# Optimization experiments

Hardware: AMD Instinct MI355X
Metric: run time of the kernel (lower is better)

Reference implementation:

```python
import jax, jax.numpy as jnp
import numpy as np

D_MODEL = 512
D_STATE = 16
D_CONV = 4
EXPAND = 2
D_INNER = EXPAND * D_MODEL  # 1024
DT_RANK = (D_MODEL + 15) // 16  # 32
BATCH = 8
SEQ = 1024
LN_EPS = 1e-5


def setup_inputs() -> dict:
    key = jax.random.key(0)
    ks = jax.random.split(key, 8)
    s = 0.02
    return {
        "x": jax.random.normal(ks[0], (BATCH, SEQ, D_MODEL), jnp.float32),
        "ln_g": jnp.ones((D_MODEL,), jnp.float32),
        "ln_b": jnp.zeros((D_MODEL,), jnp.float32),
        "in_proj_w": (jax.random.normal(ks[1], (2 * D_INNER, D_MODEL), jnp.float32) * s),
        "conv_w": (jax.random.normal(ks[2], (D_INNER, 1, D_CONV), jnp.float32) * s),
        "conv_b": jnp.zeros((D_INNER,), jnp.float32),
        "x_proj_w": (jax.random.normal(ks[3], (DT_RANK + 2 * D_STATE, D_INNER), jnp.float32) * s),
        "dt_proj_w": (jax.random.normal(ks[4], (D_INNER, DT_RANK), jnp.float32) * s),
        "dt_proj_b": jnp.full((D_INNER,), -4.0, jnp.float32),  # softplus(-4) ~ small init dt
        "A_log": jnp.log(jnp.broadcast_to(jnp.arange(1, D_STATE + 1, dtype=jnp.float32), (D_INNER, D_STATE))).copy(),
        "D": jnp.ones((D_INNER,), jnp.float32),
        "out_proj_w": (jax.random.normal(ks[5], (D_MODEL, D_INNER), jnp.float32) * s),
    }


def _block(x, ln_g, ln_b, in_proj_w, conv_w, conv_b, x_proj_w,
           dt_proj_w, dt_proj_b, A_log, D, out_proj_w):
    # Pre-norm (LayerNorm over last dim)
    mu = jnp.mean(x, axis=-1, keepdims=True)
    var = jnp.mean(jnp.square(x - mu), axis=-1, keepdims=True)
    xn = (x - mu) * jax.lax.rsqrt(var + LN_EPS) * ln_g + ln_b

    # in_proj -> (u, z), each [B, L, d_inner]
    xz = jnp.einsum('bld,ed->ble', xn, in_proj_w)
    u, z = jnp.split(xz, 2, axis=-1)

    # causal depthwise conv1d over L, then SiLU
    uc = jnp.transpose(u, (0, 2, 1))  # [B, di, L]
    uc = jax.lax.conv_general_dilated(
        uc, conv_w, window_strides=(1,), padding=[(D_CONV - 1, 0)],
        dimension_numbers=('NCH', 'OIH', 'NCH'), feature_group_count=D_INNER)
    uc = jax.nn.silu(uc + conv_b[None, :, None])
    uct = jnp.transpose(uc, (0, 2, 1))  # [B, L, di]

    # input-dependent SSM params
    x_dbl = jnp.einsum('bld,ed->ble', uct, x_proj_w)
    dt, Bt, Ct = jnp.split(x_dbl, [DT_RANK, DT_RANK + D_STATE], axis=-1)
    delta = jax.nn.softplus(jnp.einsum('blr,dr->bld', dt, dt_proj_w) + dt_proj_b)
    A = -jnp.exp(A_log)  # [di, ds]

    # selective scan over L; carry h: [B, di, ds]
    def step(h, ins):
        d_t, b_t, c_t, u_t = ins  # [B,di], [B,ds], [B,ds], [B,di]
        dA = jnp.exp(d_t[:, :, None] * A)
        h = dA * h + (d_t * u_t)[:, :, None] * b_t[:, None, :]
        y = jnp.einsum('bds,bs->bd', h, c_t)
        return h, y

    h0 = jnp.zeros((x.shape[0], D_INNER, D_STATE), x.dtype)
    xs = (jnp.swapaxes(delta, 0, 1), jnp.swapaxes(Bt, 0, 1),
          jnp.swapaxes(Ct, 0, 1), jnp.swapaxes(uct, 0, 1))
    _, ys = jax.lax.scan(step, h0, xs)
    y = jnp.swapaxes(ys, 0, 1) + uct * D  # [B, L, di]

    y = y * jax.nn.silu(z)
    out = jnp.einsum('bld,ed->ble', y, out_proj_w)
    # dropout in eval mode = identity; residual add
    return x + out


def reference(x, ln_g, ln_b, in_proj_w, conv_w, conv_b, x_proj_w,
              dt_proj_w, dt_proj_b, A_log, D, out_proj_w):
    return _block(x, ln_g, ln_b, in_proj_w, conv_w, conv_b, x_proj_w,
                  dt_proj_w, dt_proj_b, A_log, D, out_proj_w)
```

## Files before the change

### kernel.cpp

```cpp
#include <hip/hip_runtime.h>
#include <stdint.h>

#define BATCH 8
#define SEQ   1024
#define DM    512
#define DI    1024
#define DS    16
#define DTR   32
#define ROWS  (BATCH*SEQ)
#define NC    64
#define CL    16

typedef float  f32x4  __attribute__((ext_vector_type(4)));
typedef float  f32x2  __attribute__((ext_vector_type(2)));
typedef short  s16x8  __attribute__((ext_vector_type(8)));
typedef short  s16x4  __attribute__((ext_vector_type(4)));

__device__ __forceinline__ float b2f(uint16_t u) {
  union { uint32_t u; float f; } v; v.u = ((uint32_t)u) << 16; return v.f;
}
__device__ __forceinline__ uint16_t f2b(float f) {
  union { float f; uint32_t u; } v; v.f = f;
  uint32_t u = v.u;
  return (uint16_t)((u + 0x7FFFu + ((u >> 16) & 1u)) >> 16);
}

__device__ __forceinline__ void gload_lds16(const uint16_t* g, uint16_t* l) {
  __builtin_amdgcn_global_load_lds(
      (const __attribute__((address_space(1))) void*)g,
      (__attribute__((address_space(3))) void*)l, 16, 0, 0);
}

__device__ __forceinline__ void pow_tree2(float p, f32x2 a2[8]) {
  float p2 = p*p;
  f32x2 pp = {p2, p2};
  a2[0] = (f32x2){p, p2};
  a2[1] = a2[0]*pp;
  a2[2] = a2[1]*pp;
  a2[3] = a2[2]*pp;
  a2[4] = a2[3]*pp;
  a2[5] = a2[4]*pp;
  a2[6] = a2[5]*pp;
  a2[7] = a2[6]*pp;
}

#define CVT_N  ((2*DI*DM + (DTR+2*DS)*DI + DI*DTR + DM*DI)/4)
#define CVTB   (CVT_N/256)

__global__ __launch_bounds__(256) void cvt_ln(
    const float* __restrict__ s0, uint16_t* __restrict__ d0,
    const float* __restrict__ s1, uint16_t* __restrict__ d1,
    const float* __restrict__ s2, uint16_t* __restrict__ d2,
    const float* __restrict__ s3, uint16_t* __restrict__ d3,
    const float* __restrict__ x, const float* __restrict__ g,
    const float* __restrict__ bt, uint16_t* __restrict__ xn) {
  if (blockIdx.x < CVTB) {
    const int n0 = 2*DI*DM/4, n1 = (DTR+2*DS)*DI/4, n2 = DI*DTR/4;
    int i = blockIdx.x * 256 + threadIdx.x;
    const float* src; uint16_t* dst;
    if      (i < n0)          { src = s0; dst = d0; }
    else if (i < n0+n1)       { src = s1; dst = d1; i -= n0; }
    else if (i < n0+n1+n2)    { src = s2; dst = d2; i -= n0+n1; }
    else                      { src = s3; dst = d3; i -= n0+n1+n2; }
    f32x4 v = ((const f32x4*)src)[i];
    s16x4 o;
#pragma unroll
    for (int j = 0; j < 4; j++) o[j] = (short)f2b(v[j]);
    ((s16x4*)dst)[i] = o;
    return;
  }
  int w = threadIdx.x >> 6, lane = threadIdx.x & 63;
  int row = (blockIdx.x - CVTB) * 4 + w;
  const float* xr = x + (size_t)row * DM + lane * 8;
  f32x4 v0 = *(const f32x4*)xr;
  f32x4 v1 = *(const f32x4*)(xr + 4);
  float f[8]; float sacc = 0.f, sacc2 = 0.f;
#pragma unroll
  for (int i = 0; i < 4; i++) { f[i] = v0[i]; f[i+4] = v1[i]; }
#pragma unroll
  for (int i = 0; i < 8; i++) { sacc += f[i]; sacc2 += f[i]*f[i]; }
#pragma unroll
  for (int o = 32; o; o >>= 1) { sacc += __shfl_xor(sacc, o); sacc2 += __shfl_xor(sacc2, o); }
  float mu  = sacc * (1.f/DM);
  float var = sacc2 * (1.f/DM) - mu*mu;
  float rs  = rsqrtf(var + 1e-5f);
  f32x4 g0 = *(const f32x4*)(g + lane*8), g1 = *(const f32x4*)(g + lane*8 + 4);
  f32x4 b0 = *(const f32x4*)(bt + lane*8), b1 = *(const f32x4*)(bt + lane*8 + 4);
  float gg[8], bb[8];
#pragma unroll
  for (int i = 0; i < 4; i++) { gg[i] = g0[i]; gg[i+4] = g1[i]; bb[i] = b0[i]; bb[i+4] = b1[i]; }
  s16x8 o8;
#pragma unroll
  for (int i = 0; i < 8; i++) {
    float r = (f[i]-mu)*rs*gg[i] + bb[i];
    o8[i] = (short)f2b(r);
  }
  *(s16x8*)(xn + (size_t)row*DM + lane*8) = o8;
}

__device__ __forceinline__ void gemm128(
    const uint16_t* __restrict__ A, const uint16_t* __restrict__ B,
    int K, f32x4 acc[4][4], uint16_t* lA, uint16_t* lB) {
  int tid = threadIdx.x;
  int lane = tid & 63, w = tid >> 6;
  int wy = w >> 1, wx = w & 1;
  int quad = lane >> 4, l16 = lane & 15;
  int srow = tid >> 2;
  int scol = (tid & 3) ^ (srow & 3);
  const uint16_t* Ag0 = A + (size_t)(blockIdx.x*128 + srow)*K + scol*8;
  const uint16_t* Ag1 = Ag0 + (size_t)64*K;
  const uint16_t* Bg0 = B + (size_t)(blockIdx.y*128 + srow)*K + scol*8;
  const uint16_t* Bg1 = Bg0 + (size_t)64*K;
  uint16_t* lAp0 = lA + tid*8;
  uint16_t* lAp1 = lA + 2048 + tid*8;
  uint16_t* lBp0 = lB + tid*8;
  uint16_t* lBp1 = lB + 2048 + tid*8;
  int pa = quad ^ (l16 & 3);
  const uint16_t* afrag = lA + (wy*64 + l16)*32 + pa*8;
  const uint16_t* bfrag = lB + (wx*64 + l16)*32 + pa*8;
#pragma unroll
  for (int mt=0; mt<4; mt++)
#pragma unroll
  for (int nt=0; nt<4; nt++) acc[mt][nt] = (f32x4){0.f,0.f,0.f,0.f};
  for (int k0 = 0; k0 < K; k0 += 32) {
    __syncthreads();
    gload_lds16(Ag0 + k0, lAp0);
    gload_lds16(Ag1 + k0, lAp1);
    gload_lds16(Bg0 + k0, lBp0);
    gload_lds16(Bg1 + k0, lBp1);
    __syncthreads();
    s16x8 af[4], bf[4];
#pragma unroll
    for (int i=0;i<4;i++) {
      af[i] = *(const s16x8*)(afrag + i*16*32);
      bf[i] = *(const s16x8*)(bfrag + i*16*32);
    }
#pragma unroll
    for (int mt=0; mt<4; mt++)
#pragma unroll
    for (int nt=0; nt<4; nt++)
      acc[mt][nt] = __builtin_amdgcn_mfma_f32_16x16x32_bf16(af[mt], bf[nt], acc[mt][nt], 0,0,0);
  }
}

#define EPI128_IDX \
  int tid = threadIdx.x; int lane = tid & 63, w = tid >> 6; \
  int wy = w >> 1, wx = w & 1; int quad = lane >> 4, l16 = lane & 15;

__global__ __launch_bounds__(256) void gemm_inproj(
    const uint16_t* __restrict__ xn, const uint16_t* __restrict__ W,
    uint16_t* __restrict__ u, uint16_t* __restrict__ z) {
  __shared__ __align__(16) uint16_t lA[128*32];
  __shared__ __align__(16) uint16_t lB[128*32];
  f32x4 acc[4][4];
  gemm128(xn, W, DM, acc, lA, lB);
  EPI128_IDX
#pragma unroll
  for (int mt=0; mt<4; mt++)
#pragma unroll
  for (int nt=0; nt<4; nt++)
#pragma unroll
  for (int i=0; i<4; i++) {
    int gr = blockIdx.x*128 + wy*64 + mt*16 + quad*4 + i;
    int gc = blockIdx.y*128 + wx*64 + nt*16 + l16;
    float v = acc[mt][nt][i];
    if (gc < DI) u[(size_t)gr*DI + gc] = f2b(v);
    else         z[(size_t)gr*DI + (gc - DI)] = f2b(v);
  }
}

__global__ __launch_bounds__(256) void gemm_outproj(
    const uint16_t* __restrict__ yb, const uint16_t* __restrict__ W,
    const float* __restrict__ x, float* __restrict__ out) {
  __shared__ __align__(16) uint16_t lA[128*32];
  __shared__ __align__(16) uint16_t lB[128*32];
  f32x4 acc[4][4];
  gemm128(yb, W, DI, acc, lA, lB);
  EPI128_IDX
#pragma unroll
  for (int mt=0; mt<4; mt++)
#pragma unroll
  for (int nt=0; nt<4; nt++)
#pragma unroll
  for (int i=0; i<4; i++) {
    int gr = blockIdx.x*128 + wy*64 + mt*16 + quad*4 + i;
    int gc = blockIdx.y*128 + wx*64 + nt*16 + l16;
    out[(size_t)gr*DM + gc] = acc[mt][nt][i] + x[(size_t)gr*DM + gc];
  }
}

#define LSTR 40

__device__ __forceinline__ void gemm_tile(
    const uint16_t* __restrict__ A, const uint16_t* __restrict__ B,
    int ld, int kLen, int bx, f32x4 acc[2][2]) {
  __shared__ __align__(16) uint16_t lA[64*LSTR];
  __shared__ __align__(16) uint16_t lB[64*LSTR];
  int tid  = threadIdx.x;
  int lane = tid & 63, w = tid >> 6;
  int wy = w >> 1, wx = w & 1;
  int quad = lane >> 4, l16 = lane & 15;
  int sr = tid >> 2, sc = (tid & 3) << 3;
  const uint16_t* Ag = A + (size_t)(bx*64 + sr)*ld + sc;
  const uint16_t* Bg = B + (size_t)sr*ld + sc;
  uint16_t* lAw = &lA[sr*LSTR + sc];
  uint16_t* lBw = &lB[sr*LSTR + sc];
  const uint16_t* ap = &lA[(wy*32 + l16)*LSTR + quad*8];
  const uint16_t* bp = &lB[(wx*32 + l16)*LSTR + quad*8];
  f32x4 zero = {0.f,0.f,0.f,0.f};
  acc[0][0]=zero; acc[0][1]=zero; acc[1][0]=zero; acc[1][1]=zero;
  for (int k0 = 0; k0 < kLen; k0 += 32) {
    s16x8 av = *(const s16x8*)(Ag + k0);
    s16x8 bv = *(const s16x8*)(Bg + k0);
    __syncthreads();
    *(s16x8*)lAw = av;
    *(s16x8*)lBw = bv;
    __syncthreads();
    s16x8 a0 = *(const s16x8*)ap;
    s16x8 a1 = *(const s16x8*)(ap + 16*LSTR);
    s16x8 b0 = *(const s16x8*)bp;
    s16x8 b1 = *(const s16x8*)(bp + 16*LSTR);
    acc[0][0] = __builtin_amdgcn_mfma_f32_16x16x32_bf16(a0, b0, acc[0][0], 0,0,0);
    acc[0][1] = __builtin_amdgcn_mfma_f32_16x16x32_bf16(a0, b1, acc[0][1], 0,0,0);
    acc[1][0] = __builtin_amdgcn_mfma_f32_16x16x32_bf16(a1, b0, acc[1][0], 0,0,0);
    acc[1][1] = __builtin_amdgcn_mfma_f32_16x16x32_bf16(a1, b1, acc[1][1], 0,0,0);
  }
}

__global__ __launch_bounds__(256) void gemm_xproj_sk(
    const uint16_t* __restrict__ uct, const uint16_t* __restrict__ W,
    float* __restrict__ xpart) {
  f32x4 acc[2][2];
  int ks = blockIdx.y;
  gemm_tile(uct + ks*256, W + ks*256, DI, 256, blockIdx.x, acc);
  int tid = threadIdx.x; int lane = tid & 63, w = tid >> 6;
  int wy = w >> 1, wx = w & 1; int quad = lane >> 4, l16 = lane & 15;
  float* out = xpart + (size_t)ks * ROWS * 64;
#pragma unroll
  for (int mt=0; mt<2; mt++)
#pragma unroll
  for (int nt=0; nt<2; nt++)
#pragma unroll
  for (int i=0; i<4; i++) {
    int gr = blockIdx.x*64 + wy*32 + mt*16 + quad*4 + i;
    int gc = wx*32 + nt*16 + l16;
    out[(size_t)gr*64 + gc] = acc[mt][nt][i];
  }
}

__global__ __launch_bounds__(256) void gemm_dtproj_fused(
    const float* __restrict__ xpart, const uint16_t* __restrict__ W,
    const float* __restrict__ bias, uint16_t* __restrict__ delta,
    float* __restrict__ Bt, float* __restrict__ Ct) {
  __shared__ __align__(16) uint16_t lA[64*LSTR];
  __shared__ __align__(16) uint16_t lB[64*LSTR];
  int tid = threadIdx.x;
  int lane = tid & 63, w = tid >> 6;
  int wy = w >> 1, wx = w & 1;
  int quad = lane >> 4, l16 = lane & 15;
  int sr = tid >> 2, sc = (tid & 3) << 3;
  const int NX = ROWS * 64;
  {
    const float* xp = xpart + (size_t)(blockIdx.x*64 + sr)*64 + sc;
    f32x4 a0 = *(const f32x4*)xp + *(const f32x4*)(xp+NX)
             + *(const f32x4*)(xp+2*NX) + *(const f32x4*)(xp+3*NX);
    f32x4 a1 = *(const f32x4*)(xp+4) + *(const f32x4*)(xp+NX+4)
             + *(const f32x4*)(xp+2*NX+4) + *(const f32x4*)(xp+3*NX+4);
    s16x8 av;
#pragma unroll
    for (int j = 0; j < 4; j++) { av[j] = (short)f2b(a0[j]); av[4+j] = (short)f2b(a1[j]); }
    *(s16x8*)&lA[sr*LSTR + sc] = av;
    s16x8 bv = *(const s16x8*)(W + (size_t)(blockIdx.y*64 + sr)*DTR + sc);
    *(s16x8*)&lB[sr*LSTR + sc] = bv;
  }
  __syncthreads();
  const uint16_t* ap = &lA[(wy*32 + l16)*LSTR + quad*8];
  const uint16_t* bp = &lB[(wx*32 + l16)*LSTR + quad*8];
  s16x8 a0 = *(const s16x8*)ap, a1 = *(const s16x8*)(ap + 16*LSTR);
  s16x8 b0 = *(const s16x8*)bp, b1 = *(const s16x8*)(bp + 16*LSTR);
  f32x4 zero = {0.f,0.f,0.f,0.f};
  f32x4 acc[2][2];
  acc[0][0] = __builtin_amdgcn_mfma_f32_16x16x32_bf16(a0, b0, zero, 0,0,0);
  acc[0][1] = __builtin_amdgcn_mfma_f32_16x16x32_bf16(a0, b1, zero, 0,0,0);
  acc[1][0] = __builtin_amdgcn_mfma_f32_16x16x32_bf16(a1, b0, zero, 0,0,0);
  acc[1][1] = __builtin_amdgcn_mfma_f32_16x16x32_bf16(a1, b1, zero, 0,0,0);
#pragma unroll
  for (int mt=0; mt<2; mt++)
#pragma unroll
  for (int nt=0; nt<2; nt++)
#pragma unroll
  for (int i=0; i<4; i++) {
    int gr = blockIdx.x*64 + wy*32 + mt*16 + quad*4 + i;
    int gc = blockIdx.y*64 + wx*32 + nt*16 + l16;
    float v = acc[mt][nt][i] + bias[gc];
    float e  = __expf(-fabsf(v));
    float sp = fmaxf(v, 0.f) + __logf(1.f + e);
    delta[(size_t)gr*DI + gc] = f2b(sp);
  }
  if (blockIdx.y == 0) {
    int r = tid >> 2, grp = tid & 3;
    const float* xp2 = xpart + (size_t)(blockIdx.x*64 + r)*64 + 32 + grp*8;
    f32x4 v0 = *(const f32x4*)xp2 + *(const f32x4*)(xp2+NX)
             + *(const f32x4*)(xp2+2*NX) + *(const f32x4*)(xp2+3*NX);
    f32x4 v1 = *(const f32x4*)(xp2+4) + *(const f32x4*)(xp2+NX+4)
             + *(const f32x4*)(xp2+2*NX+4) + *(const f32x4*)(xp2+3*NX+4);
    size_t gr = (size_t)(blockIdx.x*64 + r);
    if (grp < 2) {
      *(f32x4*)(Bt + gr*DS + grp*8)     = v0;
      *(f32x4*)(Bt + gr*DS + grp*8 + 4) = v1;
    } else {
      *(f32x4*)(Ct + gr*DS + (grp-2)*8)     = v0;
      *(f32x4*)(Ct + gr*DS + (grp-2)*8 + 4) = v1;
    }
  }
}

__global__ __launch_bounds__(256) void conv_silu(
    const uint16_t* __restrict__ u, const float* __restrict__ cw,
    const float* __restrict__ cb, uint16_t* __restrict__ uct) {
  int idx = blockIdx.x*256 + threadIdx.x;
  int d = (idx & 255) * 4;
  int row = idx >> 8;
  int l = row & (SEQ-1);
  f32x4 wv[4];
#pragma unroll
  for (int j = 0; j < 4; j++) wv[j] = *(const f32x4*)(cw + (size_t)(d+j)*4);
  f32x4 acc = *(const f32x4*)(cb + d);
#pragma unroll
  for (int k = 0; k < 4; k++) {
    int ll = l - 3 + k;
    if (ll >= 0) {
      s16x4 uv = *(const s16x4*)(u + (size_t)(row - 3 + k)*DI + d);
#pragma unroll
      for (int j = 0; j < 4; j++) acc[j] += b2f((uint16_t)uv[j]) * wv[j][k];
    }
  }
  s16x4 o;
#pragma unroll
  for (int j = 0; j < 4; j++) {
    float sig = 1.f / (1.f + __expf(-acc[j]));
    o[j] = (short)f2b(acc[j] * sig);
  }
  *(s16x4*)(uct + (size_t)row*DI + d) = o;
}


__global__ __launch_bounds__(256) void scan_pass1(
    const uint16_t* __restrict__ delta, const uint16_t* __restrict__ uct,
    const float* __restrict__ Bt,
    float* __restrict__ prun, uint16_t* __restrict__ Hc) {
  int b = blockIdx.x, c = blockIdx.y;
  int tid = threadIdx.x;
  int d = blockIdx.z * 256 + tid;
  __shared__ __align__(16) float lB[CL*DS];
  if (tid < CL*DS/4)
    ((f32x4*)lB)[tid] = ((const f32x4*)(Bt + (size_t)(b*SEQ + c*CL)*DS))[tid];
  float p_run = 1.f;
  f32x2 h2[8];
#pragma unroll
  for (int k = 0; k < 8; k++) h2[k] = (f32x2){0.f, 0.f};
  size_t r0 = ((size_t)(b*SEQ + c*CL))*DI + d;
  float dv_n = b2f(delta[r0]);
  float uv_n = b2f(uct[r0]);
  __syncthreads();
  for (int t = 0; t < CL; t++) {
    float dv = dv_n, uv = uv_n;
    int tn = (t + 1 < CL) ? (t + 1) : t;
    dv_n = b2f(delta[r0 + (size_t)tn*DI]);
    uv_n = b2f(uct[r0 + (size_t)tn*DI]);
    float du = dv * uv;
    f32x2 du2 = {du, du};
    float p = __expf(-dv);
    f32x2 a2[8];
    pow_tree2(p, a2);
    p_run *= p;
    const f32x4* bq4 = (const f32x4*)(lB + t*DS);
    f32x4 bA = bq4[0], bB = bq4[1], bC = bq4[2], bD = bq4[3];
    f32x2 bb[8] = {{bA[0],bA[1]},{bA[2],bA[3]},{bB[0],bB[1]},{bB[2],bB[3]},
                   {bC[0],bC[1]},{bC[2],bC[3]},{bD[0],bD[1]},{bD[2],bD[3]}};
#pragma unroll
    for (int k = 0; k < 8; k++)
      h2[k] = a2[k]*h2[k] + du2*bb[k];
  }
  prun[((size_t)(b*NC + c))*DI + d] = p_run;
  size_t obase = ((size_t)(b*NC + c)*DS)*DI + d;
#pragma unroll
  for (int k = 0; k < 8; k++) {
    Hc[obase + (size_t)(2*k  )*DI] = f2b(h2[k][0]);
    Hc[obase + (size_t)(2*k+1)*DI] = f2b(h2[k][1]);
  }
}

__global__ __launch_bounds__(256) void scan_pass2(
    const float* __restrict__ prun, const uint16_t* __restrict__ Hc,
    uint16_t* __restrict__ Hinit) {
  int gid = blockIdx.x * 256 + threadIdx.x;
  int d = gid & (DI-1);
  int bs = gid >> 10;
  int b = bs >> 4, s = bs & (DS-1);
  int e = s + 1;
  float H = 0.f;
  size_t pbase = ((size_t)b*NC)*DI + d;
  size_t hbase = ((size_t)b*NC*DS + s)*DI + d;
  float    p_n = prun[pbase];
  uint16_t h_n = Hc[hbase];
  for (int c = 0; c < NC; c++) {
    float p = p_n; uint16_t hraw = h_n;
    int cn = (c + 1 < NC) ? (c + 1) : c;
    p_n = prun[pbase + (size_t)cn*DI];
    h_n = Hc[hbase + (size_t)cn*DS*DI];
    float r = 1.f, q = p;
    if (e & 1)  r *= q; q *= q;
    if (e & 2)  r *= q; q *= q;
    if (e & 4)  r *= q; q *= q;
    if (e & 8)  r *= q; q *= q;
    if (e & 16) r *= q;
    size_t hidx = hbase + (size_t)c*DS*DI;
    Hinit[hidx] = f2b(H);
    H = r * H + b2f(hraw);
  }
}

__global__ __launch_bounds__(256) void scan_pass3(
    const uint16_t* __restrict__ delta, const uint16_t* __restrict__ uct,
    const uint16_t* __restrict__ z, const float* __restrict__ Bt,
    const float* __restrict__ Ct,
    const float* __restrict__ Dp, const uint16_t* __restrict__ Hinit,
    uint16_t* __restrict__ y) {
  int b = blockIdx.x, c = blockIdx.y;
  int tid = threadIdx.x;
  int d = blockIdx.z * 256 + tid;
  __shared__ __align__(16) float lB[CL*DS];
  __shared__ __align__(16) float lC[CL*DS];
  if (tid < CL*DS/4)
    ((f32x4*)lB)[tid] = ((const f32x4*)(Bt + (size_t)(b*SEQ + c*CL)*DS))[tid];
  else if (tid < CL*DS/2)
    ((f32x4*)lC)[tid - CL*DS/4] = ((const f32x4*)(Ct + (size_t)(b*SEQ + c*CL)*DS))[tid - CL*DS/4];
  float Dd = Dp[d];
  f32x2 h2[8];
  size_t ibase = ((size_t)(b*NC + c)*DS)*DI + d;
#pragma unroll
  for (int k = 0; k < 8; k++) {
    h2[k][0] = b2f(Hinit[ibase + (size_t)(2*k  )*DI]);
    h2[k][1] = b2f(Hinit[ibase + (size_t)(2*k+1)*DI]);
  }
  size_t r0 = ((size_t)(b*SEQ + c*CL))*DI + d;
  float dv_n = b2f(delta[r0]);
  float uv_n = b2f(uct[r0]);
  float zv_n = b2f(z[r0]);
  __syncthreads();
  for (int t = 0; t < CL; t++) {
    float dv = dv_n, uv = uv_n, zv = zv_n;
    int tn = (t + 1 < CL) ? (t + 1) : t;
    dv_n = b2f(delta[r0 + (size_t)tn*DI]);
    uv_n = b2f(uct[r0 + (size_t)tn*DI]);
    zv_n = b2f(z[r0 + (size_t)tn*DI]);
    float du = dv * uv;
    f32x2 du2 = {du, du};
    float p = __expf(-dv);
    f32x2 a2[8];
    pow_tree2(p, a2);
    const f32x4* bq4 = (const f32x4*)(lB + t*DS);
    const f32x4* cq4 = (const f32x4*)(lC + t*DS);
    f32x4 bA = bq4[0], bB = bq4[1], bC = bq4[2], bD = bq4[3];
    f32x4 cA = cq4[0], cB = cq4[1], cC = cq4[2], cD = cq4[3];
    f32x2 bb[8] = {{bA[0],bA[1]},{bA[2],bA[3]},{bB[0],bB[1]},{bB[2],bB[3]},
                   {bC[0],bC[1]},{bC[2],bC[3]},{bD[0],bD[1]},{bD[2],bD[3]}};
    f32x2 cc[8] = {{cA[0],cA[1]},{cA[2],cA[3]},{cB[0],cB[1]},{cB[2],cB[3]},
                   {cC[0],cC[1]},{cC[2],cC[3]},{cD[0],cD[1]},{cD[2],cD[3]}};
    f32x2 yv2 = {0.f, 0.f};
#pragma unroll
    for (int k = 0; k < 8; k++) {
      h2[k] = a2[k]*h2[k] + du2*bb[k];
      yv2 = yv2 + h2[k]*cc[k];
    }
    float yv = yv2[0] + yv2[1];
    yv = (yv + uv * Dd) * (zv / (1.f + __expf(-zv)));
    y[r0 + (size_t)t*DI] = f2b(yv);
  }
}

extern "C" void kernel_launch(void* const* d_in, const int* in_sizes, int n_in,
                              void* d_out, int out_size, void* d_ws, size_t ws_size,
                              hipStream_t stream) {
  const float* x        = (const float*)d_in[0];
  const float* ln_g     = (const float*)d_in[1];
  const float* ln_b     = (const float*)d_in[2];
  const float* in_projW = (const float*)d_in[3];
  const float* conv_w   = (const float*)d_in[4];
  const float* conv_b   = (const float*)d_in[5];
  const float* x_projW  = (const float*)d_in[6];
  const float* dt_projW = (const float*)d_in[7];
  const float* dt_projB = (const float*)d_in[8];
  const float* Dp       = (const float*)d_in[10];
  const float* out_projW= (const float*)d_in[11];

  char* ws = (char*)d_ws;
  size_t off = 0;
  auto alloc = [&](size_t bytes) { void* p = ws + off; off += (bytes + 255) & ~255ull; return p; };
  uint16_t* xn  = (uint16_t*)alloc((size_t)ROWS*DM*2);
  uint16_t* u   = (uint16_t*)alloc((size_t)ROWS*DI*2);
  uint16_t* z   = (uint16_t*)alloc((size_t)ROWS*DI*2);
  uint16_t* uct = (uint16_t*)alloc((size_t)ROWS*DI*2);
  float*    Btb = (float*)   alloc((size_t)ROWS*DS*4);
  float*    Ctb = (float*)   alloc((size_t)ROWS*DS*4);
  uint16_t* yb  = (uint16_t*)alloc((size_t)ROWS*DI*2);
  uint16_t* wIn = (uint16_t*)alloc((size_t)2*DI*DM*2);
  uint16_t* wX  = (uint16_t*)alloc((size_t)(DTR+2*DS)*DI*2);
  uint16_t* wDt = (uint16_t*)alloc((size_t)DI*DTR*2);
  uint16_t* wOut= (uint16_t*)alloc((size_t)DM*DI*2);
  float*    prun = (float*)   alloc((size_t)BATCH*NC*DI*4);
  uint16_t* Hc   = (uint16_t*)alloc((size_t)BATCH*NC*DS*DI*2);
  uint16_t* Hini = (uint16_t*)alloc((size_t)BATCH*NC*DS*DI*2);
  float*    xpart = (float*)alloc((size_t)4*ROWS*64*4);
  uint16_t* delta = u;

  cvt_ln          <<<CVTB + ROWS/4, 256, 0, stream>>>(
      in_projW, wIn, x_projW, wX, dt_projW, wDt, out_projW, wOut,
      x, ln_g, ln_b, xn);
  gemm_inproj     <<<dim3(ROWS/128, (2*DI)/128), 256, 0, stream>>>(xn, wIn, u, z);
  conv_silu       <<<(ROWS*DI/4)/256, 256, 0, stream>>>(u, conv_w, conv_b, uct);
  gemm_xproj_sk   <<<dim3(ROWS/64, 4), 256, 0, stream>>>(uct, wX, xpart);
  gemm_dtproj_fused<<<dim3(ROWS/64, DI/64), 256, 0, stream>>>(
      xpart, wDt, dt_projB, delta, Btb, Ctb);
  scan_pass1      <<<dim3(BATCH, NC, DI/256), 256, 0, stream>>>(delta, uct, Btb, prun, Hc);
  scan_pass2      <<<(BATCH*DS*DI)/256, 256, 0, stream>>>(prun, Hc, Hini);
  scan_pass3      <<<dim3(BATCH, NC, DI/256), 256, 0, stream>>>(delta, uct, z, Btb, Ctb, Dp, Hini, yb);
  gemm_outproj    <<<dim3(ROWS/128, DM/128), 256, 0, stream>>>(yb, wOut, x, (float*)d_out);
}
```

Before: 239.0 us.

## Fuse causal conv+SiLU into x_proj GEMM and scan passes; lengthen scan chunks

Drops the standalone conv_silu kernel and the materialized uct buffer. The conv+SiLU is now recomputed from u inside the x_proj GEMM's A-tile load and inside scan_pass1/pass3 using a rolling 3-tap window. This removes a full write and several reads of a ROWS×DI bf16 tensor. The cost is extra ALU and exp work in the GEMM and scans, plus redundant loads of previous rows. Delta now gets its own buffer instead of aliasing u, and the scan chunking changes from 64×16 to 32×32, which halves the scan grid parallelism but shortens the inter-chunk pass.

```diff
diff --git a/kernel.cpp b/kernel.cpp
--- a/kernel.cpp
+++ b/kernel.cpp
@@ -8,8 +8,8 @@
 #define DS    16
 #define DTR   32
 #define ROWS  (BATCH*SEQ)
-#define NC    64
-#define CL    16
+#define NC    32
+#define CL    32
 
 typedef float  f32x4  __attribute__((ext_vector_type(4)));
 typedef float  f32x2  __attribute__((ext_vector_type(2)));
@@ -191,9 +191,10 @@
 
 #define LSTR 40
 
-__device__ __forceinline__ void gemm_tile(
-    const uint16_t* __restrict__ A, const uint16_t* __restrict__ B,
-    int ld, int kLen, int bx, f32x4 acc[2][2]) {
+__global__ __launch_bounds__(256) void gemm_xproj_sk(
+    const uint16_t* __restrict__ u, const float* __restrict__ cw,
+    const float* __restrict__ cb, const uint16_t* __restrict__ W,
+    float* __restrict__ xpart) {
   __shared__ __align__(16) uint16_t lA[64*LSTR];
   __shared__ __align__(16) uint16_t lB[64*LSTR];
   int tid  = threadIdx.x;
@@ -201,40 +202,54 @@
   int wy = w >> 1, wx = w & 1;
   int quad = lane >> 4, l16 = lane & 15;
   int sr = tid >> 2, sc = (tid & 3) << 3;
-  const uint16_t* Ag = A + (size_t)(bx*64 + sr)*ld + sc;
-  const uint16_t* Bg = B + (size_t)sr*ld + sc;
+  int ks = blockIdx.y;
+  int grow = blockIdx.x*64 + sr;
+  int l = grow & (SEQ-1);
+  const uint16_t* Ag = u + (size_t)grow*DI + ks*256 + sc;
+  const uint16_t* Bg = W + (size_t)sr*DI + ks*256 + sc;
   uint16_t* lAw = &lA[sr*LSTR + sc];
   uint16_t* lBw = &lB[sr*LSTR + sc];
   const uint16_t* ap = &lA[(wy*32 + l16)*LSTR + quad*8];
   const uint16_t* bp = &lB[(wx*32 + l16)*LSTR + quad*8];
   f32x4 zero = {0.f,0.f,0.f,0.f};
+  f32x4 acc[2][2];
   acc[0][0]=zero; acc[0][1]=zero; acc[1][0]=zero; acc[1][1]=zero;
-  for (int k0 = 0; k0 < kLen; k0 += 32) {
-    s16x8 av = *(const s16x8*)(Ag + k0);
+  s16x8 z8;
+#pragma unroll
+  for (int j = 0; j < 8; j++) z8[j] = 0;
+  for (int k0 = 0; k0 < 256; k0 += 32) {
+    int col0 = ks*256 + k0 + sc;
+    s16x8 a3 = *(const s16x8*)(Ag + k0);
+    s16x8 a0v = z8, a1v = z8, a2v = z8;
+    if (l >= 3) a0v = *(const s16x8*)(Ag + k0 - 3*DI);
+    if (l >= 2) a1v = *(const s16x8*)(Ag + k0 - 2*DI);
+    if (l >= 1) a2v = *(const s16x8*)(Ag + k0 - DI);
     s16x8 bv = *(const s16x8*)(Bg + k0);
+    f32x4 cb0 = *(const f32x4*)(cb + col0);
+    f32x4 cb1 = *(const f32x4*)(cb + col0 + 4);
+    s16x8 av;
+#pragma unroll
+    for (int j = 0; j < 8; j++) {
+      f32x4 wj = *(const f32x4*)(cw + (size_t)(col0 + j)*4);
+      float ca = (j < 4 ? cb0[j] : cb1[j-4])
+               + wj[0]*b2f((uint16_t)a0v[j]) + wj[1]*b2f((uint16_t)a1v[j])
+               + wj[2]*b2f((uint16_t)a2v[j]) + wj[3]*b2f((uint16_t)a3[j]);
+      float uv = ca / (1.f + __expf(-ca));
+      av[j] = (short)f2b(uv);
+    }
     __syncthreads();
     *(s16x8*)lAw = av;
     *(s16x8*)lBw = bv;
     __syncthreads();
-    s16x8 a0 = *(const s16x8*)ap;
-    s16x8 a1 = *(const s16x8*)(ap + 16*LSTR);
-    s16x8 b0 = *(const s16x8*)bp;
-    s16x8 b1 = *(const s16x8*)(bp + 16*LSTR);
-    acc[0][0] = __builtin_amdgcn_mfma_f32_16x16x32_bf16(a0, b0, acc[0][0], 0,0,0);
-    acc[0][1] = __builtin_amdgcn_mfma_f32_16x16x32_bf16(a0, b1, acc[0][1], 0,0,0);
-    acc[1][0] = __builtin_amdgcn_mfma_f32_16x16x32_bf16(a1, b0, acc[1][0], 0,0,0);
-    acc[1][1] = __builtin_amdgcn_mfma_f32_16x16x32_bf16(a1, b1, acc[1][1], 0,0,0);
-  }
-}
-
-__global__ __launch_bounds__(256) void gemm_xproj_sk(
-    const uint16_t* __restrict__ uct, const uint16_t* __restrict__ W,
-    float* __restrict__ xpart) {
-  f32x4 acc[2][2];
-  int ks = blockIdx.y;
-  gemm_tile(uct + ks*256, W + ks*256, DI, 256, blockIdx.x, acc);
-  int tid = threadIdx.x; int lane = tid & 63, w = tid >> 6;
-  int wy = w >> 1, wx = w & 1; int quad = lane >> 4, l16 = lane & 15;
+    s16x8 fa0 = *(const s16x8*)ap;
+    s16x8 fa1 = *(const s16x8*)(ap + 16*LSTR);
+    s16x8 fb0 = *(const s16x8*)bp;
+    s16x8 fb1 = *(const s16x8*)(bp + 16*LSTR);
+    acc[0][0] = __builtin_amdgcn_mfma_f32_16x16x32_bf16(fa0, fb0, acc[0][0], 0,0,0);
+    acc[0][1] = __builtin_amdgcn_mfma_f32_16x16x32_bf16(fa0, fb1, acc[0][1], 0,0,0);
+    acc[1][0] = __builtin_amdgcn_mfma_f32_16x16x32_bf16(fa1, fb0, acc[1][0], 0,0,0);
+    acc[1][1] = __builtin_amdgcn_mfma_f32_16x16x32_bf16(fa1, fb1, acc[1][1], 0,0,0);
+  }
   float* out = xpart + (size_t)ks * ROWS * 64;
 #pragma unroll
   for (int mt=0; mt<2; mt++)
@@ -315,38 +330,10 @@
   }
 }
 
-__global__ __launch_bounds__(256) void conv_silu(
-    const uint16_t* __restrict__ u, const float* __restrict__ cw,
-    const float* __restrict__ cb, uint16_t* __restrict__ uct) {
-  int idx = blockIdx.x*256 + threadIdx.x;
-  int d = (idx & 255) * 4;
-  int row = idx >> 8;
-  int l = row & (SEQ-1);
-  f32x4 wv[4];
-#pragma unroll
-  for (int j = 0; j < 4; j++) wv[j] = *(const f32x4*)(cw + (size_t)(d+j)*4);
-  f32x4 acc = *(const f32x4*)(cb + d);
-#pragma unroll
-  for (int k = 0; k < 4; k++) {
-    int ll = l - 3 + k;
-    if (ll >= 0) {
-      s16x4 uv = *(const s16x4*)(u + (size_t)(row - 3 + k)*DI + d);
-#pragma unroll
-      for (int j = 0; j < 4; j++) acc[j] += b2f((uint16_t)uv[j]) * wv[j][k];
-    }
-  }
-  s16x4 o;
-#pragma unroll
-  for (int j = 0; j < 4; j++) {
-    float sig = 1.f / (1.f + __expf(-acc[j]));
-    o[j] = (short)f2b(acc[j] * sig);
-  }
-  *(s16x4*)(uct + (size_t)row*DI + d) = o;
-}
-
 
 __global__ __launch_bounds__(256) void scan_pass1(
-    const uint16_t* __restrict__ delta, const uint16_t* __restrict__ uct,
+    const uint16_t* __restrict__ delta, const uint16_t* __restrict__ u,
+    const float* __restrict__ cw, const float* __restrict__ cb,
     const float* __restrict__ Bt,
     float* __restrict__ prun, uint16_t* __restrict__ Hc) {
   int b = blockIdx.x, c = blockIdx.y;
@@ -355,19 +342,30 @@
   __shared__ __align__(16) float lB[CL*DS];
   if (tid < CL*DS/4)
     ((f32x4*)lB)[tid] = ((const f32x4*)(Bt + (size_t)(b*SEQ + c*CL)*DS))[tid];
+  f32x4 wv = *(const f32x4*)(cw + (size_t)d*4);
+  float cbd = cb[d];
   float p_run = 1.f;
   f32x2 h2[8];
 #pragma unroll
   for (int k = 0; k < 8; k++) h2[k] = (f32x2){0.f, 0.f};
   size_t r0 = ((size_t)(b*SEQ + c*CL))*DI + d;
+  float uw0 = 0.f, uw1 = 0.f, uw2 = 0.f;
+  if (c > 0) {
+    uw0 = b2f(u[r0 - 3*(size_t)DI]);
+    uw1 = b2f(u[r0 - 2*(size_t)DI]);
+    uw2 = b2f(u[r0 -   (size_t)DI]);
+  }
   float dv_n = b2f(delta[r0]);
-  float uv_n = b2f(uct[r0]);
+  float un_n = b2f(u[r0]);
   __syncthreads();
   for (int t = 0; t < CL; t++) {
-    float dv = dv_n, uv = uv_n;
+    float dv = dv_n, u3 = un_n;
     int tn = (t + 1 < CL) ? (t + 1) : t;
     dv_n = b2f(delta[r0 + (size_t)tn*DI]);
-    uv_n = b2f(uct[r0 + (size_t)tn*DI]);
+    un_n = b2f(u[r0 + (size_t)tn*DI]);
+    float ca = cbd + wv[0]*uw0 + wv[1]*uw1 + wv[2]*uw2 + wv[3]*u3;
+    float uv = ca / (1.f + __expf(-ca));
+    uw0 = uw1; uw1 = uw2; uw2 = u3;
     float du = dv * uv;
     f32x2 du2 = {du, du};
     float p = __expf(-dv);
@@ -422,7 +420,8 @@
 }
 
 __global__ __launch_bounds__(256) void scan_pass3(
-    const uint16_t* __restrict__ delta, const uint16_t* __restrict__ uct,
+    const uint16_t* __restrict__ delta, const uint16_t* __restrict__ u,
+    const float* __restrict__ cw, const float* __restrict__ cb,
     const uint16_t* __restrict__ z, const float* __restrict__ Bt,
     const float* __restrict__ Ct,
     const float* __restrict__ Dp, const uint16_t* __restrict__ Hinit,
@@ -436,6 +435,8 @@
     ((f32x4*)lB)[tid] = ((const f32x4*)(Bt + (size_t)(b*SEQ + c*CL)*DS))[tid];
   else if (tid < CL*DS/2)
     ((f32x4*)lC)[tid - CL*DS/4] = ((const f32x4*)(Ct + (size_t)(b*SEQ + c*CL)*DS))[tid - CL*DS/4];
+  f32x4 wv = *(const f32x4*)(cw + (size_t)d*4);
+  float cbd = cb[d];
   float Dd = Dp[d];
   f32x2 h2[8];
   size_t ibase = ((size_t)(b*NC + c)*DS)*DI + d;
@@ -445,16 +446,25 @@
     h2[k][1] = b2f(Hinit[ibase + (size_t)(2*k+1)*DI]);
   }
   size_t r0 = ((size_t)(b*SEQ + c*CL))*DI + d;
+  float uw0 = 0.f, uw1 = 0.f, uw2 = 0.f;
+  if (c > 0) {
+    uw0 = b2f(u[r0 - 3*(size_t)DI]);
+    uw1 = b2f(u[r0 - 2*(size_t)DI]);
+    uw2 = b2f(u[r0 -   (size_t)DI]);
+  }
   float dv_n = b2f(delta[r0]);
-  float uv_n = b2f(uct[r0]);
+  float un_n = b2f(u[r0]);
   float zv_n = b2f(z[r0]);
   __syncthreads();
   for (int t = 0; t < CL; t++) {
-    float dv = dv_n, uv = uv_n, zv = zv_n;
+    float dv = dv_n, u3 = un_n, zv = zv_n;
     int tn = (t + 1 < CL) ? (t + 1) : t;
     dv_n = b2f(delta[r0 + (size_t)tn*DI]);
-    uv_n = b2f(uct[r0 + (size_t)tn*DI]);
+    un_n = b2f(u[r0 + (size_t)tn*DI]);
     zv_n = b2f(z[r0 + (size_t)tn*DI]);
+    float ca = cbd + wv[0]*uw0 + wv[1]*uw1 + wv[2]*uw2 + wv[3]*u3;
+    float uv = ca / (1.f + __expf(-ca));
+    uw0 = uw1; uw1 = uw2; uw2 = u3;
     float du = dv * uv;
     f32x2 du2 = {du, du};
     float p = __expf(-dv);
@@ -501,7 +511,7 @@
   uint16_t* xn  = (uint16_t*)alloc((size_t)ROWS*DM*2);
   uint16_t* u   = (uint16_t*)alloc((size_t)ROWS*DI*2);
   uint16_t* z   = (uint16_t*)alloc((size_t)ROWS*DI*2);
-  uint16_t* uct = (uint16_t*)alloc((size_t)ROWS*DI*2);
+  uint16_t* delta = (uint16_t*)alloc((size_t)ROWS*DI*2);
   float*    Btb = (float*)   alloc((size_t)ROWS*DS*4);
   float*    Ctb = (float*)   alloc((size_t)ROWS*DS*4);
   uint16_t* yb  = (uint16_t*)alloc((size_t)ROWS*DI*2);
@@ -513,18 +523,18 @@
   uint16_t* Hc   = (uint16_t*)alloc((size_t)BATCH*NC*DS*DI*2);
   uint16_t* Hini = (uint16_t*)alloc((size_t)BATCH*NC*DS*DI*2);
   float*    xpart = (float*)alloc((size_t)4*ROWS*64*4);
-  uint16_t* delta = u;
 
   cvt_ln          <<<CVTB + ROWS/4, 256, 0, stream>>>(
       in_projW, wIn, x_projW, wX, dt_projW, wDt, out_projW, wOut,
       x, ln_g, ln_b, xn);
   gemm_inproj     <<<dim3(ROWS/128, (2*DI)/128), 256, 0, stream>>>(xn, wIn, u, z);
-  conv_silu       <<<(ROWS*DI/4)/256, 256, 0, stream>>>(u, conv_w, conv_b, uct);
-  gemm_xproj_sk   <<<dim3(ROWS/64, 4), 256, 0, stream>>>(uct, wX, xpart);
+  gemm_xproj_sk   <<<dim3(ROWS/64, 4), 256, 0, stream>>>(u, conv_w, conv_b, wX, xpart);
   gemm_dtproj_fused<<<dim3(ROWS/64, DI/64), 256, 0, stream>>>(
       xpart, wDt, dt_projB, delta, Btb, Ctb);
-  scan_pass1      <<<dim3(BATCH, NC, DI/256), 256, 0, stream>>>(delta, uct, Btb, prun, Hc);
+  scan_pass1      <<<dim3(BATCH, NC, DI/256), 256, 0, stream>>>(
+      delta, u, conv_w, conv_b, Btb, prun, Hc);
   scan_pass2      <<<(BATCH*DS*DI)/256, 256, 0, stream>>>(prun, Hc, Hini);
-  scan_pass3      <<<dim3(BATCH, NC, DI/256), 256, 0, stream>>>(delta, uct, z, Btb, Ctb, Dp, Hini, yb);
+  scan_pass3      <<<dim3(BATCH, NC, DI/256), 256, 0, stream>>>(
+      delta, u, conv_w, conv_b, z, Btb, Ctb, Dp, Hini, yb);
   gemm_outproj    <<<dim3(ROWS/128, DM/128), 256, 0, stream>>>(yb, wOut, x, (float*)d_out);
 }
```

Measured after the change: 234.6 us. Within noise of the previous version (-1.8%).
